# Kernel tuning notes

Measured on AMD Instinct MI355X. Metric: run time of the kernel, lower is better.

The kernel has to match this reference:

```python
import jax, jax.numpy as jnp
import numpy as np

B, H, W = 2, 256, 256
PTS, IMP = 64, 64
FOCAL = 4.2
NEAR, FAR = 0.1, 2.0


def _camera_dirs():
    x, y = jnp.meshgrid(jnp.linspace(1.0, -1.0, H, dtype=jnp.float32),
                        jnp.linspace(1.0, -1.0, W, dtype=jnp.float32), indexing='xy')
    return jnp.stack([x / FOCAL, y / FOCAL, jnp.ones_like(x)], -1).reshape(-1, 3)  # (H*W,3)


def _exclusive_prod(x):
    cp = jnp.cumprod(x, axis=-1)
    return jnp.concatenate([jnp.ones_like(cp[..., :1]), cp[..., :-1]], axis=-1)


def _ray_marching(op, vals):
    # op (R,P), vals (R,P,C)  -> nerfacc.exclusive_prod + accumulate_along_rays
    absorption = _exclusive_prod(1.0 - op)
    w = op * absorption
    accum_vals = jnp.einsum('rp,rpc->rc', w, vals)
    accum_op = jnp.clip(jnp.sum(w, -1, keepdims=True), 0.0, 1.0)
    return accum_vals, accum_op, w


def _sample_cdf(depth_vals, cdfs, n):
    # inverse-transform importance sampling (nerfacc.importance_sampling, stratified=False)
    # depth_vals, cdfs: (R,P) -> bin edges (R, n+1)
    u = jnp.linspace(0.0, 1.0, n + 1, dtype=depth_vals.dtype)
    u = jnp.broadcast_to(u, (depth_vals.shape[0], n + 1))
    inds = jax.vmap(lambda c, uu: jnp.searchsorted(c, uu, side='right'))(cdfs, u)
    below = jnp.clip(inds - 1, 0, cdfs.shape[-1] - 1)
    above = jnp.clip(inds, 0, cdfs.shape[-1] - 1)
    cdf0 = jnp.take_along_axis(cdfs, below, -1)
    cdf1 = jnp.take_along_axis(cdfs, above, -1)
    d0 = jnp.take_along_axis(depth_vals, below, -1)
    d1 = jnp.take_along_axis(depth_vals, above, -1)
    denom = jnp.where(cdf1 - cdf0 < 1e-8, 1.0, cdf1 - cdf0)
    t = jnp.clip((u - cdf0) / denom, 0.0, 1.0)
    return d0 + t * (d1 - d0)


def _query(coords, dirs, W_query):
    # stand-in nerf_query_fn: tiny linear head (coords,dirs)->(opacity, rgb)
    d = jnp.broadcast_to(dirs[:, None, :], coords.shape)
    feat = jnp.concatenate([coords, d], -1) @ W_query  # (R,P,4)
    return jax.nn.sigmoid(feat[..., 0]), jax.nn.sigmoid(feat[..., 1:4])


def _two_path_render(transform_matrix, W_query):
    cam = _camera_dirs()                                   # (HW,3)
    Rm = transform_matrix[:, :, :3]                        # (B,3,3)
    t = transform_matrix[:, :, 3]                          # (B,3)
    dirs = jnp.einsum('bij,nj->bni', Rm, cam).reshape(-1, 3)   # (R,3)
    origins = jnp.broadcast_to(t[:, None, :], (B, H * W, 3)).reshape(-1, 3)
    n_rays = dirs.shape[0]
    depths = jnp.broadcast_to(jnp.linspace(NEAR, FAR, PTS, dtype=jnp.float32), (n_rays, PTS))
    coords = origins[:, None, :] + depths[..., None] * dirs[:, None, :]
    # coarse pass
    c_op, c_vals = _query(coords, dirs, W_query)
    c_accum_vals, c_accum_op, w = _ray_marching(c_op, c_vals)
    # CDF importance resampling
    wpad = w + 1e-5
    cdfs = jnp.cumsum(wpad / jnp.sum(wpad, -1, keepdims=True), -1)
    bins = _sample_cdf(depths, cdfs, IMP)                  # (R, IMP+1)
    f_depths = 0.5 * (bins[..., :-1] + bins[..., 1:])
    f_coords = origins[:, None, :] + f_depths[..., None] * dirs[:, None, :]
    # fine pass
    f_op, f_vals = _query(f_coords, dirs, W_query)
    # hierarchical sort-merge
    d_all = jnp.concatenate([depths, f_depths], -1)
    v_all = jnp.concatenate([c_vals, f_vals], -2)
    o_all = jnp.concatenate([c_op, f_op], -1)
    idx = jnp.argsort(d_all, -1)
    d_all = jnp.take_along_axis(d_all, idx, -1)
    o_all = jnp.take_along_axis(o_all, idx, -1)
    v_all = jnp.take_along_axis(v_all, idx[..., None], -2)
    f_accum_vals, f_accum_op, w2 = _ray_marching(o_all, v_all)
    ray_depths = jnp.einsum('rp,rp->r', w2, d_all)[:, None]
    ray_depths = ray_depths + (1.0 - f_accum_op) * d_all.max()
    ray_depths = (ray_depths - ray_depths.min()) / (ray_depths.max() - ray_depths.min())
    shp = (B, H, W, -1)
    c_img = c_accum_vals.reshape(shp).transpose(0, 3, 1, 2)
    f_img = f_accum_vals.reshape(shp).transpose(0, 3, 1, 2)
    d_img = ray_depths.reshape(shp).transpose(0, 3, 1, 2)
    return c_img, f_img, d_img


def setup_inputs() -> dict:
    key = jax.random.key(0)
    k1, k2 = jax.random.split(key)
    transform_matrix = jax.random.normal(k1, (B, 3, 4), dtype=jnp.float32)
    W_query = jax.random.normal(k2, (6, 4), dtype=jnp.float32) * 0.5
    return {'transform_matrix': transform_matrix, 'W_query': W_query}


def reference(transform_matrix, W_query):
    return _two_path_render(transform_matrix, W_query)
```

## Files before the change

### kernel.cpp

```cpp
#include <hip/hip_runtime.h>
#include <math.h>


#define NT 64
#define PTS 64
#define NRAYS (2*256*256)
#define NEARV 0.1f
#define STEPV (1.9f/63.0f)
#define FAR63 (0.1f + 63.0f*(1.9f/63.0f))
#define NL2E (-1.4426950408889634f)
#define ECLAMP 1.0e37f

__global__ __launch_bounds__(NT, 2) void nerf_main(
    const float* __restrict__ tm, const float* __restrict__ wq,
    float* __restrict__ out, unsigned int* __restrict__ bmm)
{
    __shared__ float fd[PTS + 1][NT];
    const int tid = threadIdx.x;
    const int r = blockIdx.x * NT + tid;
    const int b = r >> 16, n = r & 65535;
    const int i = n >> 8, j = n & 255;

    float bA[4], sA[4];
    {
        float cx = (1.0f + (float)j * (-2.0f/255.0f)) * (1.0f/4.2f);
        float cy = (1.0f + (float)i * (-2.0f/255.0f)) * (1.0f/4.2f);
        const float* tmb = tm + b*12;
        float dx = tmb[0]*cx + tmb[1]*cy + tmb[2];
        float dy = tmb[4]*cx + tmb[5]*cy + tmb[6];
        float dz = tmb[8]*cx + tmb[9]*cy + tmb[10];
        float ox = tmb[3], oy = tmb[7], oz = tmb[11];
        #pragma unroll
        for (int c = 0; c < 4; c++) {
            float s  = dx*wq[0*4+c] + dy*wq[1*4+c] + dz*wq[2*4+c];
            float bv = ox*wq[0*4+c] + oy*wq[1*4+c] + oz*wq[2*4+c]
                     + dx*wq[3*4+c] + dy*wq[4*4+c] + dz*wq[5*4+c];
            sA[c] = s * NL2E;
            bA[c] = bv * NL2E;
        }
    }

    float eV[4], kV[4], e00;
    #pragma unroll
    for (int c = 0; c < 4; c++) {
        eV[c] = __builtin_amdgcn_exp2f(bA[c] + NEARV*sA[c]);
        kV[c] = __builtin_amdgcn_exp2f(sA[c]*STEPV);
    }
    e00 = eV[0];

    float T = 1.0f, S = 0.0f;
    float a0 = 0.0f, a1 = 0.0f, a2 = 0.0f;
    #pragma unroll 4
    for (int p = 0; p < PTS; p++) {
        float e0c = fminf(eV[0], ECLAMP);
        float r0 = __builtin_amdgcn_rcpf(1.0f + e0c);
        float m0 = e0c * r0;
        float v0 = __builtin_amdgcn_rcpf(1.0f + eV[1]);
        float v1 = __builtin_amdgcn_rcpf(1.0f + eV[2]);
        float v2 = __builtin_amdgcn_rcpf(1.0f + eV[3]);
        eV[0] *= kV[0];
        eV[1] *= kV[1];
        eV[2] *= kV[2];
        eV[3] *= kV[3];
        float w = r0 * T;
        a0 = fmaf(w, v0, a0);
        a1 = fmaf(w, v1, a1);
        a2 = fmaf(w, v2, a2);
        S += w;
        T *= m0;
    }
    S += 64.0f * 1e-5f;
    out[(b*3+0)*65536 + n] = a0;
    out[(b*3+1)*65536 + n] = a1;
    out[(b*3+2)*65536 + n] = a2;

    float Sinv = __builtin_amdgcn_rcpf(S);
    float op0  = __builtin_amdgcn_rcpf(1.0f + e00);
    float T2   = 1.0f - op0;
    float c_lo = 0.0f;
    float c_hi = (op0 + 1e-5f) * Sinv;
    int ind = 0, wslot = 0;
    float u = 0.015625f;
    float bin_prev = NEARV;
    float eP  = e00 * kV[0];
    float opn = __builtin_amdgcn_rcpf(1.0f + eP);
    #pragma unroll 2
    for (int it = 0; it < 2*PTS; it++) {
        float eP2  = eP * kV[0];
        float opnB = __builtin_amdgcn_rcpf(1.0f + eP2);
        bool adv = (ind < PTS) && (c_hi <= u);
        float wn  = opn * T2;
        float d0  = fmaf((float)(ind - 1), STEPV, NEARV);
        float den = c_hi - c_lo;
        den = (den < 1e-8f) ? 1.0f : den;
        float t = (u - c_lo) * __builtin_amdgcn_rcpf(den);
        t = fminf(fmaxf(t, 0.0f), 1.0f);
        float bin = fmaf(t, STEPV, d0);
        bin = (ind <= 0)   ? NEARV : bin;
        bin = (ind >= PTS) ? FAR63 : bin;
        float fdep = 0.5f * (bin_prev + bin);
        int widx = adv ? PTS : wslot;
        fd[widx][tid] = fdep;
        float nc_hi = c_hi + (wn + 1e-5f) * Sinv;
        float nT2   = T2 * (1.0f - opn);
        bool advm   = adv && (ind < 62);
        c_lo     = adv ? c_hi : c_lo;
        c_hi     = adv ? nc_hi : c_hi;
        T2       = adv ? nT2 : T2;
        bin_prev = adv ? bin_prev : bin;
        eP  = advm ? eP2  : eP;
        opn = advm ? opnB : opn;
        ind += adv ? 1 : 0;
        u  += adv ? 0.0f : 0.015625f;
        wslot = adv ? wslot : min(wslot + 1, PTS);
    }

    const float bA0 = bA[0], sA0 = sA[0], bA1 = bA[1], sA1 = sA[1];
    const float bA2 = bA[2], sA2 = sA[2], bA3 = bA[3], sA3 = sA[3];
    float T3 = 1.0f, sw = 0.0f, rd = 0.0f;
    float f0 = 0.0f, f1 = 0.0f, f2 = 0.0f;
    int pc = 0, pf = 0;
    float dc = NEARV;
    float cur = fd[0][tid], nxt = fd[1][tid];
    float tmp = fd[2][tid];
    #pragma unroll 2
    for (int it = 0; it < 2*PTS; it++) {
        float pend = tmp;
        float dfv = (pf < PTS) ? cur : 3.0e38f;
        bool tc = (pc < PTS) && (dc <= dfv);
        float d = tc ? dc : dfv;
        pc += tc ? 1 : 0;
        dc = fmaf((float)pc, STEPV, NEARV);
        cur = tc ? cur : nxt;
        nxt = tc ? nxt : pend;
        pf += tc ? 0 : 1;
        tmp = fd[min(pf + 2, PTS)][tid];
        float e0 = __builtin_amdgcn_exp2f(fmaf(d, sA0, bA0));
        float e1 = __builtin_amdgcn_exp2f(fmaf(d, sA1, bA1));
        float e2 = __builtin_amdgcn_exp2f(fmaf(d, sA2, bA2));
        float e3 = __builtin_amdgcn_exp2f(fmaf(d, sA3, bA3));
        float e0c = fminf(e0, ECLAMP);
        float r0 = __builtin_amdgcn_rcpf(1.0f + e0c);
        float m0 = e0c * r0;
        float v0 = __builtin_amdgcn_rcpf(1.0f + e1);
        float v1 = __builtin_amdgcn_rcpf(1.0f + e2);
        float v2 = __builtin_amdgcn_rcpf(1.0f + e3);
        float w = r0 * T3;
        f0 = fmaf(w, v0, f0);
        f1 = fmaf(w, v1, f1);
        f2 = fmaf(w, v2, f2);
        sw += w;
        rd  = fmaf(w, d, rd);
        T3 *= m0;
    }

    out[393216 + (b*3+0)*65536 + n] = f0;
    out[393216 + (b*3+1)*65536 + n] = f1;
    out[393216 + (b*3+2)*65536 + n] = f2;
    float fop  = fminf(fmaxf(sw, 0.0f), 1.0f);
    float rdep = rd + (1.0f - fop) * 2.0f;
    out[786432 + r] = rdep;

    unsigned ub  = __float_as_uint(rdep);
    unsigned kmn = ub;
    unsigned kmx = ~ub;
    #pragma unroll
    for (int m = 32; m >= 1; m >>= 1) {
        unsigned omn = (unsigned)__shfl_xor((int)kmn, m, 64);
        unsigned omx = (unsigned)__shfl_xor((int)kmx, m, 64);
        kmn = (omn < kmn) ? omn : kmn;
        kmx = (omx < kmx) ? omx : kmx;
    }
    if (tid == 0) {
        bmm[2*blockIdx.x + 0] = kmn;
        bmm[2*blockIdx.x + 1] = kmx;
    }
}

__global__ __launch_bounds__(256) void nerf_norm(float* __restrict__ out,
                                                 const unsigned int* __restrict__ bmm)
{
    const int tid = threadIdx.x;
    unsigned kmn = 0xFFFFFFFFu, kmx = 0xFFFFFFFFu;
    const uint2* bm2 = (const uint2*)bmm;
    #pragma unroll
    for (int t = 0; t < 8; t++) {
        uint2 p = bm2[tid + 256*t];
        kmn = min(kmn, p.x);
        kmx = min(kmx, p.y);
    }
    #pragma unroll
    for (int m = 32; m >= 1; m >>= 1) {
        unsigned omn = (unsigned)__shfl_xor((int)kmn, m, 64);
        unsigned omx = (unsigned)__shfl_xor((int)kmx, m, 64);
        kmn = (omn < kmn) ? omn : kmn;
        kmx = (omx < kmx) ? omx : kmx;
    }
    __shared__ unsigned smn[4], smx[4];
    if ((tid & 63) == 0) { smn[tid >> 6] = kmn; smx[tid >> 6] = kmx; }
    __syncthreads();
    kmn = min(min(smn[0], smn[1]), min(smn[2], smn[3]));
    kmx = min(min(smx[0], smx[1]), min(smx[2], smx[3]));
    float mn = __uint_as_float(kmn);
    float mx = __uint_as_float(~kmx);
    int idx = blockIdx.x * 256 + tid;
    float v = out[786432 + idx];
    out[786432 + idx] = (v - mn) * __builtin_amdgcn_rcpf(mx - mn);
}

extern "C" void kernel_launch(void* const* d_in, const int* in_sizes, int n_in,
                              void* d_out, int out_size, void* d_ws, size_t ws_size,
                              hipStream_t stream) {
    (void)in_sizes; (void)n_in; (void)out_size; (void)ws_size;
    const float* tm = (const float*)d_in[0];
    const float* wq = (const float*)d_in[1];
    float* out = (float*)d_out;
    unsigned int* bmm = (unsigned int*)d_ws;
    nerf_main<<<NRAYS/NT, NT, 0, stream>>>(tm, wq, out, bmm);
    nerf_norm<<<NRAYS/256, 256, 0, stream>>>(out, bmm);
}
```

Before: 104.5 us.

## Split each ray's marching across two threads and combine partial transmittance sums

Each ray is now handled by two threads. Each thread marches half of the coarse samples, and half of the merged coarse-plus-fine samples, located by a binary search for the merge split point. The partial transmittance and accumulations are combined with lane shuffles. The serial importance-sampling CDF walk still runs on only the first 64 threads of each block, using values passed through shared memory. This shortens the per-thread serial chain at the cost of extra syncs, shared-memory staging and idle threads during the CDF phase.

```diff
diff --git a/kernel.cpp b/kernel.cpp
--- a/kernel.cpp
+++ b/kernel.cpp
@@ -2,7 +2,7 @@
 #include <math.h>
 
 
-#define NT 64
+#define NT 128
 #define PTS 64
 #define NRAYS (2*256*256)
 #define NEARV 0.1f
@@ -11,13 +11,17 @@
 #define NL2E (-1.4426950408889634f)
 #define ECLAMP 1.0e37f
 
-__global__ __launch_bounds__(NT, 2) void nerf_main(
+__global__ __launch_bounds__(NT, 4) void nerf_main(
     const float* __restrict__ tm, const float* __restrict__ wq,
     float* __restrict__ out, unsigned int* __restrict__ bmm)
 {
-    __shared__ float fd[PTS + 1][NT];
+    __shared__ float fd[PTS + 1][64];
+    __shared__ float sE00[64], sKV0[64], sSinv[64];
+    __shared__ unsigned smn2[2], smx2[2];
     const int tid = threadIdx.x;
-    const int r = blockIdx.x * NT + tid;
+    const int rl  = tid >> 1;
+    const int h   = tid & 1;
+    const int r   = blockIdx.x * 64 + rl;
     const int b = r >> 16, n = r & 65535;
     const int i = n >> 8, j = n & 255;
 
@@ -40,18 +44,19 @@
         }
     }
 
-    float eV[4], kV[4], e00;
+    float kV[4], eV[4];
+    float e00 = __builtin_amdgcn_exp2f(bA[0] + NEARV*sA[0]);
+    float dstart = h ? fmaf(32.0f, STEPV, NEARV) : NEARV;
     #pragma unroll
     for (int c = 0; c < 4; c++) {
-        eV[c] = __builtin_amdgcn_exp2f(bA[c] + NEARV*sA[c]);
         kV[c] = __builtin_amdgcn_exp2f(sA[c]*STEPV);
-    }
-    e00 = eV[0];
-
-    float T = 1.0f, S = 0.0f;
+        eV[c] = __builtin_amdgcn_exp2f(bA[c] + dstart*sA[c]);
+    }
+
+    float T = 1.0f, Sw = 0.0f;
     float a0 = 0.0f, a1 = 0.0f, a2 = 0.0f;
     #pragma unroll 4
-    for (int p = 0; p < PTS; p++) {
+    for (int p = 0; p < 32; p++) {
         float e0c = fminf(eV[0], ECLAMP);
         float r0 = __builtin_amdgcn_rcpf(1.0f + e0c);
         float m0 = e0c * r0;
@@ -66,65 +71,102 @@
         a0 = fmaf(w, v0, a0);
         a1 = fmaf(w, v1, a1);
         a2 = fmaf(w, v2, a2);
-        S += w;
+        Sw += w;
         T *= m0;
     }
-    S += 64.0f * 1e-5f;
-    out[(b*3+0)*65536 + n] = a0;
-    out[(b*3+1)*65536 + n] = a1;
-    out[(b*3+2)*65536 + n] = a2;
-
-    float Sinv = __builtin_amdgcn_rcpf(S);
-    float op0  = __builtin_amdgcn_rcpf(1.0f + e00);
-    float T2   = 1.0f - op0;
-    float c_lo = 0.0f;
-    float c_hi = (op0 + 1e-5f) * Sinv;
-    int ind = 0, wslot = 0;
-    float u = 0.015625f;
-    float bin_prev = NEARV;
-    float eP  = e00 * kV[0];
-    float opn = __builtin_amdgcn_rcpf(1.0f + eP);
-    #pragma unroll 2
-    for (int it = 0; it < 2*PTS; it++) {
-        float eP2  = eP * kV[0];
-        float opnB = __builtin_amdgcn_rcpf(1.0f + eP2);
-        bool adv = (ind < PTS) && (c_hi <= u);
-        float wn  = opn * T2;
-        float d0  = fmaf((float)(ind - 1), STEPV, NEARV);
-        float den = c_hi - c_lo;
-        den = (den < 1e-8f) ? 1.0f : den;
-        float t = (u - c_lo) * __builtin_amdgcn_rcpf(den);
-        t = fminf(fmaxf(t, 0.0f), 1.0f);
-        float bin = fmaf(t, STEPV, d0);
-        bin = (ind <= 0)   ? NEARV : bin;
-        bin = (ind >= PTS) ? FAR63 : bin;
-        float fdep = 0.5f * (bin_prev + bin);
-        int widx = adv ? PTS : wslot;
-        fd[widx][tid] = fdep;
-        float nc_hi = c_hi + (wn + 1e-5f) * Sinv;
-        float nT2   = T2 * (1.0f - opn);
-        bool advm   = adv && (ind < 62);
-        c_lo     = adv ? c_hi : c_lo;
-        c_hi     = adv ? nc_hi : c_hi;
-        T2       = adv ? nT2 : T2;
-        bin_prev = adv ? bin_prev : bin;
-        eP  = advm ? eP2  : eP;
-        opn = advm ? opnB : opn;
-        ind += adv ? 1 : 0;
-        u  += adv ? 0.0f : 0.015625f;
-        wslot = adv ? wslot : min(wslot + 1, PTS);
-    }
-
+    float oT = __shfl_xor(T, 1, 64);
+    float oS = __shfl_xor(Sw, 1, 64);
+    float o0 = __shfl_xor(a0, 1, 64);
+    float o1 = __shfl_xor(a1, 1, 64);
+    float o2 = __shfl_xor(a2, 1, 64);
+    float T_mid = h ? oT : T;
+    float Sfull = (h ? oS : Sw) + T_mid * (h ? Sw : oS) + 64.0f*1e-5f;
+    float A0 = (h ? o0 : a0) + T_mid * (h ? a0 : o0);
+    float A1 = (h ? o1 : a1) + T_mid * (h ? a1 : o1);
+    float A2 = (h ? o2 : a2) + T_mid * (h ? a2 : o2);
+    if (h == 0) {
+        out[(b*3+0)*65536 + n] = A0;
+        out[(b*3+1)*65536 + n] = A1;
+        out[(b*3+2)*65536 + n] = A2;
+        sE00[rl]  = e00;
+        sKV0[rl]  = kV[0];
+        sSinv[rl] = __builtin_amdgcn_rcpf(Sfull);
+    }
+    __syncthreads();
+
+    if (tid < 64) {
+        const int q = tid;
+        float e0q = sE00[q];
+        float kq  = sKV0[q];
+        float Siq = sSinv[q];
+        float op0 = __builtin_amdgcn_rcpf(1.0f + e0q);
+        float T2   = 1.0f - op0;
+        float c_lo = 0.0f;
+        float c_hi = (op0 + 1e-5f) * Siq;
+        int ind = 0, wslot = 0;
+        float u = 0.015625f;
+        float bin_prev = NEARV;
+        float eP  = e0q * kq;
+        float opn = __builtin_amdgcn_rcpf(1.0f + eP);
+        #pragma unroll 2
+        for (int it = 0; it < 2*PTS; it++) {
+            float eP2  = eP * kq;
+            float opnB = __builtin_amdgcn_rcpf(1.0f + eP2);
+            bool adv = (ind < PTS) && (c_hi <= u);
+            float wn  = opn * T2;
+            float d0  = fmaf((float)(ind - 1), STEPV, NEARV);
+            float den = c_hi - c_lo;
+            den = (den < 1e-8f) ? 1.0f : den;
+            float t = (u - c_lo) * __builtin_amdgcn_rcpf(den);
+            t = fminf(fmaxf(t, 0.0f), 1.0f);
+            float bin = fmaf(t, STEPV, d0);
+            bin = (ind <= 0)   ? NEARV : bin;
+            bin = (ind >= PTS) ? FAR63 : bin;
+            float fdep = 0.5f * (bin_prev + bin);
+            int widx = adv ? PTS : wslot;
+            fd[widx][q] = fdep;
+            float nc_hi = c_hi + (wn + 1e-5f) * Siq;
+            float nT2   = T2 * (1.0f - opn);
+            bool advm   = adv && (ind < 62);
+            c_lo     = adv ? c_hi : c_lo;
+            c_hi     = adv ? nc_hi : c_hi;
+            T2       = adv ? nT2 : T2;
+            bin_prev = adv ? bin_prev : bin;
+            eP  = advm ? eP2  : eP;
+            opn = advm ? opnB : opn;
+            ind += adv ? 1 : 0;
+            u  += adv ? 0.0f : 0.015625f;
+            wslot = adv ? wslot : min(wslot + 1, PTS);
+        }
+    }
+    __syncthreads();
+
+    int pc, pf;
+    if (h) {
+        int lo = 0, hi = 64;
+        #pragma unroll
+        for (int s = 0; s < 7; s++) {
+            int mid = (lo + hi + 1) >> 1;
+            float cd = fmaf((float)(mid - 1), STEPV, NEARV);
+            float fv = fd[64 - mid][rl];
+            bool p = (mid == 0) || (cd <= fv);
+            lo = p ? mid : lo;
+            hi = p ? hi : mid - 1;
+        }
+        pc = lo; pf = 64 - lo;
+    } else {
+        pc = 0; pf = 0;
+    }
     const float bA0 = bA[0], sA0 = sA[0], bA1 = bA[1], sA1 = sA[1];
     const float bA2 = bA[2], sA2 = sA[2], bA3 = bA[3], sA3 = sA[3];
+    float dc  = fmaf((float)pc, STEPV, NEARV);
+    float cur = fd[min(pf, PTS)][rl];
+    float nxt = fd[min(pf + 1, PTS)][rl];
+    float tmp = fd[min(pf + 2, PTS)][rl];
     float T3 = 1.0f, sw = 0.0f, rd = 0.0f;
     float f0 = 0.0f, f1 = 0.0f, f2 = 0.0f;
-    int pc = 0, pf = 0;
-    float dc = NEARV;
-    float cur = fd[0][tid], nxt = fd[1][tid];
-    float tmp = fd[2][tid];
     #pragma unroll 2
-    for (int it = 0; it < 2*PTS; it++) {
+    for (int it = 0; it < PTS; it++) {
         float pend = tmp;
         float dfv = (pf < PTS) ? cur : 3.0e38f;
         bool tc = (pc < PTS) && (dc <= dfv);
@@ -134,7 +176,7 @@
         cur = tc ? cur : nxt;
         nxt = tc ? nxt : pend;
         pf += tc ? 0 : 1;
-        tmp = fd[min(pf + 2, PTS)][tid];
+        tmp = fd[min(pf + 2, PTS)][rl];
         float e0 = __builtin_amdgcn_exp2f(fmaf(d, sA0, bA0));
         float e1 = __builtin_amdgcn_exp2f(fmaf(d, sA1, bA1));
         float e2 = __builtin_amdgcn_exp2f(fmaf(d, sA2, bA2));
@@ -153,13 +195,26 @@
         rd  = fmaf(w, d, rd);
         T3 *= m0;
     }
-
-    out[393216 + (b*3+0)*65536 + n] = f0;
-    out[393216 + (b*3+1)*65536 + n] = f1;
-    out[393216 + (b*3+2)*65536 + n] = f2;
-    float fop  = fminf(fmaxf(sw, 0.0f), 1.0f);
-    float rdep = rd + (1.0f - fop) * 2.0f;
-    out[786432 + r] = rdep;
+    float q3 = __shfl_xor(T3, 1, 64);
+    float qs = __shfl_xor(sw, 1, 64);
+    float q0 = __shfl_xor(f0, 1, 64);
+    float q1 = __shfl_xor(f1, 1, 64);
+    float q2 = __shfl_xor(f2, 1, 64);
+    float qr = __shfl_xor(rd, 1, 64);
+    float TA  = h ? q3 : T3;
+    float swF = (h ? qs : sw) + TA * (h ? sw : qs);
+    float f0F = (h ? q0 : f0) + TA * (h ? f0 : q0);
+    float f1F = (h ? q1 : f1) + TA * (h ? f1 : q1);
+    float f2F = (h ? q2 : f2) + TA * (h ? f2 : q2);
+    float rdF = (h ? qr : rd) + TA * (h ? rd : qr);
+    float fop  = fminf(fmaxf(swF, 0.0f), 1.0f);
+    float rdep = rdF + (1.0f - fop) * 2.0f;
+    if (h == 0) {
+        out[393216 + (b*3+0)*65536 + n] = f0F;
+        out[393216 + (b*3+1)*65536 + n] = f1F;
+        out[393216 + (b*3+2)*65536 + n] = f2F;
+        out[786432 + r] = rdep;
+    }
 
     unsigned ub  = __float_as_uint(rdep);
     unsigned kmn = ub;
@@ -171,9 +226,11 @@
         kmn = (omn < kmn) ? omn : kmn;
         kmx = (omx < kmx) ? omx : kmx;
     }
+    if ((tid & 63) == 0) { smn2[tid >> 6] = kmn; smx2[tid >> 6] = kmx; }
+    __syncthreads();
     if (tid == 0) {
-        bmm[2*blockIdx.x + 0] = kmn;
-        bmm[2*blockIdx.x + 1] = kmx;
+        bmm[2*blockIdx.x + 0] = min(smn2[0], smn2[1]);
+        bmm[2*blockIdx.x + 1] = min(smx2[0], smx2[1]);
     }
 }
 
@@ -216,6 +273,6 @@
     const float* wq = (const float*)d_in[1];
     float* out = (float*)d_out;
     unsigned int* bmm = (unsigned int*)d_ws;
-    nerf_main<<<NRAYS/NT, NT, 0, stream>>>(tm, wq, out, bmm);
+    nerf_main<<<NRAYS/64, NT, 0, stream>>>(tm, wq, out, bmm);
     nerf_norm<<<NRAYS/256, 256, 0, stream>>>(out, bmm);
 }
```

New measurement: 109.8 us. +5.1%, slower.
